# Kernel tuning notes

Hardware: AMD Instinct MI355X
Metric: run time of the kernel (lower is better)

Reference implementation:

```python
import jax, jax.numpy as jnp
import numpy as np

NUM_ITER = 3  # num_itterations

def squash(s):
    # Faithful to the module's (non-standard) squash: out = |s|^2 * s / (1 + |s|^2 * (|s| + 1e-9)).
    # torch sums over dim=-2 of [..., D, 1]; here s is [..., D] so sum over last axis.
    sq = jnp.sum(s * s, axis=-1, keepdims=True)
    norm = jnp.sqrt(sq)
    return sq * s / (1.0 + sq * (norm + 1e-9))

def setup_inputs() -> dict:
    key = jax.random.key(0)
    k1, k2 = jax.random.split(key)
    B, P, N, T, D = 512, 1152, 10, 16, 8
    x = jax.random.normal(k1, (B, P, D), dtype=jnp.float32)          # input capsules
    W = jax.random.normal(k2, (P, N, T, D), dtype=jnp.float32)       # routing transform (torch W with leading 1 dropped)
    return {"x": x, "W": W}

def reference(x, B_unused=None, *, _=None, **__):
    raise RuntimeError('placeholder')

def reference(x, W):
    # prediction u_hat[b,p,n,:] = W[p,n] @ x[b,p]  -> [B, P, N, T]
    pred = jnp.einsum('pntd,bpd->bpnt', W, x)
    B, P, N = pred.shape[0], pred.shape[1], pred.shape[2]
    b_ij = jnp.zeros((B, P, N), dtype=x.dtype)
    v = None
    for i in range(NUM_ITER):
        # torch.tensor(c_ij) detaches the coupling coefficients from the graph
        c = jax.lax.stop_gradient(jax.nn.softmax(b_ij, axis=2))      # softmax over next-caps dim
        s = jnp.einsum('bpn,bpnt->bnt', c, pred)                     # weighted sum over prev caps
        v = squash(s)                                                # [B, N, T]
        if i < NUM_ITER - 1:
            a = jnp.einsum('bpnt,bnt->bpn', pred, v)                 # agreement
            b_ij = b_ij + jnp.mean(a, axis=0, keepdims=True)         # torch mean over batch, keepdim, broadcast-add
    return v[..., None]  # [B, numNextCaps, nextCapsDim, 1] matching torch v_j.squeeze(1)
```

## Files before the change

kernel.cpp:

```cpp
#include <hip/hip_runtime.h>
#include <hip/hip_bf16.h>


typedef __attribute__((ext_vector_type(8))) short bfrag;
typedef __attribute__((ext_vector_type(4))) float f32x4;

constexpr int B_ = 512, P_ = 1152, N_ = 10, NT_ = 160;
constexpr int K1_ = 9216, NKC_ = 288;

__device__ __forceinline__ unsigned short f2bf(float f) {
    unsigned u = __float_as_uint(f);
    return (unsigned short)((u + 0x7fffu + ((u >> 16) & 1u)) >> 16);
}
__device__ __forceinline__ float bf2f(unsigned short s) {
    return __uint_as_float((unsigned)s << 16);
}
__device__ __forceinline__ bfrag mkfrag(f32x4 a, f32x4 b, float c) {
    bfrag f;
    f[0] = (short)f2bf(a.x * c); f[1] = (short)f2bf(a.y * c);
    f[2] = (short)f2bf(a.z * c); f[3] = (short)f2bf(a.w * c);
    f[4] = (short)f2bf(b.x * c); f[5] = (short)f2bf(b.y * c);
    f[6] = (short)f2bf(b.z * c); f[7] = (short)f2bf(b.w * c);
    return f;
}

__global__ __launch_bounds__(256) void k_prep(const float* __restrict__ x,
                                              const float* __restrict__ W,
                                              unsigned short* __restrict__ Xb,
                                              unsigned short* __restrict__ Xga,
                                              unsigned short* __restrict__ Wc,
                                              unsigned short* __restrict__ Wb) {
    const int bid = blockIdx.x, tid = threadIdx.x;
    const int w = tid >> 6, ln = tid & 63, col = ln & 15, q = ln >> 4;
    if (bid < 1152) {
        __shared__ unsigned short tile[64][72];
        const int pd0 = (bid >> 3) * 64, b0 = (bid & 7) * 64;
        const int c0 = tid & 63, r0 = tid >> 6;
#pragma unroll
        for (int i = 0; i < 16; ++i) {
            const int br = i * 4 + r0;
            tile[c0][br] = f2bf(x[(size_t)(b0 + br) * K1_ + pd0 + c0]);
        }
        __syncthreads();
#pragma unroll
        for (int fi = 0; fi < 2; ++fi) {
            const int f = w + fi * 4;
            const int pdblk_l = f & 3, kc_l = f >> 2;
            bfrag fr;
#pragma unroll
            for (int j = 0; j < 8; ++j)
                fr[j] = (short)tile[pdblk_l * 16 + col][kc_l * 32 + q * 8 + j];
            const size_t addr = ((size_t)(((pd0 >> 4) + pdblk_l) * 16 + (b0 >> 5) + kc_l)) * 512 + ln * 8;
            *(bfrag*)(Xga + addr) = fr;
        }
#pragma unroll
        for (int fi = 0; fi < 2; ++fi) {
            const int f = w + fi * 4;
            const int mblk_l = f & 3, kc_l = f >> 2;
            bfrag fr;
#pragma unroll
            for (int j = 0; j < 8; ++j)
                fr[j] = (short)tile[kc_l * 32 + q * 8 + j][mblk_l * 16 + col];
            const size_t addr = ((size_t)(((b0 >> 4) + mblk_l) * NKC_ + (pd0 >> 5) + kc_l)) * 512 + ln * 8;
            *(bfrag*)(Xb + addr) = fr;
        }
    } else if (bid < 1872) {
        const int task = (bid - 1152) * 4 + w;
        const int n = task / NKC_, kc = task % NKC_;
        const int p = kc * 4 + q;
        const float* wr = W + ((size_t)p * NT_ + n * 16 + col) * 8;
        const bfrag f = mkfrag(*(const f32x4*)wr, *(const f32x4*)(wr + 4), 0.1f);
        *(bfrag*)(Wc + ((size_t)(n * NKC_ + kc)) * 512 + ln * 8) = f;
    } else {
        const int idx = (bid - 1872) * 256 + tid;
        const int p = ((idx >> 6) * 16 + (idx & 15)) >> 3, d = idx & 7;
        const int q2 = (idx & 63) >> 4;
        unsigned short* dst = Wb + (size_t)idx * 40;
#pragma unroll
        for (int mt = 0; mt < N_; ++mt)
#pragma unroll
            for (int r = 0; r < 4; ++r)
                dst[mt * 4 + r] = f2bf(W[((size_t)p * NT_ + mt * 16 + q2 * 4 + r) * 8 + d]);
    }
}

__global__ __launch_bounds__(1024) void k_sv(const unsigned short* __restrict__ Xb,
                                             const unsigned short* __restrict__ Wc,
                                             unsigned short* __restrict__ Vt,
                                             float* __restrict__ outp,
                                             int final_it) {
    __shared__ float red[15 * 256];
    const int tid = threadIdx.x;
    const int w = tid >> 6, lane = tid & 63, col = lane & 15, q = lane >> 4;
    const int mblk = blockIdx.x;
    const int n0 = blockIdx.y;

    f32x4 accA = (f32x4){0.f, 0.f, 0.f, 0.f};
    f32x4 accB = (f32x4){0.f, 0.f, 0.f, 0.f};
    const int kc0 = w * 18;
    const unsigned short* Xp = Xb + ((size_t)(mblk * NKC_ + kc0)) * 512 + lane * 8;
    const unsigned short* W0 = Wc + ((size_t)(n0 * NKC_ + kc0)) * 512 + lane * 8;
#pragma unroll 3
    for (int i = 0; i < 9; ++i) {
        const bfrag a0 = *(const bfrag*)Xp;
        const bfrag b0 = *(const bfrag*)W0;
        const bfrag a1 = *(const bfrag*)(Xp + 512);
        const bfrag b1 = *(const bfrag*)(W0 + 512);
        accA = __builtin_amdgcn_mfma_f32_16x16x32_bf16(a0, b0, accA, 0, 0, 0);
        accB = __builtin_amdgcn_mfma_f32_16x16x32_bf16(a1, b1, accB, 0, 0, 0);
        Xp += 1024; W0 += 1024;
    }
    f32x4 acc;
#pragma unroll
    for (int r = 0; r < 4; ++r) acc[r] = accA[r] + accB[r];
    if (w) {
#pragma unroll
        for (int r = 0; r < 4; ++r)
            red[(w - 1) * 256 + r * 64 + q * 16 + col] = acc[r];
    }
    __syncthreads();
    if (w == 0) {
#pragma unroll
        for (int r = 0; r < 4; ++r) {
            const int li = r * 64 + q * 16 + col;
            float s = acc[r];
#pragma unroll
            for (int j = 0; j < 15; ++j) s += red[j * 256 + li];
            float sq = s * s;
            sq += __shfl_xor(sq, 1);
            sq += __shfl_xor(sq, 2);
            sq += __shfl_xor(sq, 4);
            sq += __shfl_xor(sq, 8);
            const float norm = sqrtf(sq);
            const float scale = sq / (1.0f + sq * (norm + 1e-9f));
            const float vv = s * scale;
            const int b = mblk * 16 + q * 4 + r;
            const int nt = n0 * 16 + col;
            if (final_it) outp[(size_t)b * NT_ + nt] = vv;
            else          Vt[(size_t)nt * B_ + b] = f2bf(vv);
        }
    }
}

__global__ __launch_bounds__(256) void k_ga(const unsigned short* __restrict__ Vt,
                                            const unsigned short* __restrict__ Xga,
                                            const unsigned short* __restrict__ Wb,
                                            const float* __restrict__ W,
                                            float* __restrict__ bbar,
                                            unsigned short* __restrict__ Wc,
                                            int accum) {
    __shared__ float bred[3][64][41];
    __shared__ float csm[2][N_];
    const int tid = threadIdx.x;
    const int w = tid >> 6, lane = tid & 63, col = lane & 15, q = lane >> 4;
    const int pdblk = blockIdx.x;
    const int p = (pdblk * 16 + col) >> 3, d = col & 7;

    f32x4 acc[N_];
#pragma unroll
    for (int mt = 0; mt < N_; ++mt) acc[mt] = (f32x4){0.f, 0.f, 0.f, 0.f};

    const int kb0 = w * 4;
#pragma unroll
    for (int kc = kb0; kc < kb0 + 4; ++kc) {
        const bfrag bf = *(const bfrag*)(Xga + ((size_t)(pdblk * 16 + kc)) * 512 + lane * 8);
#pragma unroll
        for (int mt = 0; mt < N_; ++mt) {
            const bfrag af = *(const bfrag*)(Vt + (size_t)(mt * 16 + col) * B_ + kc * 32 + q * 8);
            acc[mt] = __builtin_amdgcn_mfma_f32_16x16x32_bf16(af, bf, acc[mt], 0, 0, 0);
        }
    }
    if (w) {
#pragma unroll
        for (int mt = 0; mt < N_; ++mt)
#pragma unroll
            for (int r = 0; r < 4; ++r)
                bred[w - 1][lane][mt * 4 + r] = acc[mt][r];
    }
    __syncthreads();
    if (w == 0) {
        unsigned short wv[40];
        const unsigned short* ws2 = Wb + ((size_t)(pdblk * 64 + lane)) * 40;
#pragma unroll
        for (int v = 0; v < 40; ++v) wv[v] = ws2[v];
        float part[N_];
#pragma unroll
        for (int mt = 0; mt < N_; ++mt) {
            float s = 0.f;
#pragma unroll
            for (int r = 0; r < 4; ++r) {
                const float h = acc[mt][r] + bred[0][lane][mt * 4 + r]
                              + bred[1][lane][mt * 4 + r] + bred[2][lane][mt * 4 + r];
                s = fmaf(bf2f(wv[mt * 4 + r]), h, s);
            }
            s += __shfl_xor(s, 1);
            s += __shfl_xor(s, 2);
            s += __shfl_xor(s, 4);
            s += __shfl_xor(s, 16);
            s += __shfl_xor(s, 32);
            part[mt] = s;
        }
        if (q == 0 && d == 0) {
            const int pl = col >> 3;
            float bv[N_];
#pragma unroll
            for (int mt = 0; mt < N_; ++mt) {
                bv[mt] = part[mt] * (1.0f / 512.0f);
                if (accum) bv[mt] += bbar[(size_t)p * N_ + mt];
                bbar[(size_t)p * N_ + mt] = bv[mt];
            }
            float m = -1e30f;
#pragma unroll
            for (int mt = 0; mt < N_; ++mt) m = fmaxf(m, bv[mt]);
            float sum = 0.f;
#pragma unroll
            for (int mt = 0; mt < N_; ++mt) { bv[mt] = __expf(bv[mt] - m); sum += bv[mt]; }
            const float inv = 1.f / sum;
#pragma unroll
            for (int mt = 0; mt < N_; ++mt) csm[pl][mt] = bv[mt] * inv;
        }
    }
    __syncthreads();
    const int p0 = pdblk * 2;
#pragma unroll
    for (int task = tid; task < 320; task += 256) {
        const int pl = task / 160, rem = task % 160;
        const int n = rem >> 4, cl = rem & 15;
        const int pp = p0 + pl;
        const float c = csm[pl][n];
        const float* wr = W + ((size_t)pp * NT_ + n * 16 + cl) * 8;
        const size_t addr = ((size_t)(n * NKC_ + (pp >> 2))) * 512 + (pp & 3) * 128 + cl * 8;
        *(bfrag*)(Wc + addr) = mkfrag(*(const f32x4*)wr, *(const f32x4*)(wr + 4), c);
    }
}

extern "C" void kernel_launch(void* const* d_in, const int* in_sizes, int n_in,
                              void* d_out, int out_size, void* d_ws, size_t ws_size,
                              hipStream_t stream) {
    const float* x = (const float*)d_in[0];
    const float* W = (const float*)d_in[1];

    char* wsp = (char*)d_ws;
    float* bbar = (float*)wsp;
    unsigned short* Xb  = (unsigned short*)(wsp + 46080);
    unsigned short* Xga = Xb + (size_t)32 * NKC_ * 512;
    unsigned short* Wc  = Xga + (size_t)576 * 16 * 512;
    unsigned short* Wb  = Wc + (size_t)N_ * NKC_ * 512;
    unsigned short* Vt  = Wb + (size_t)576 * 64 * 40;
    float* outp = (float*)d_out;

    k_prep<<<dim3(2016), dim3(256), 0, stream>>>(x, W, Xb, Xga, Wc, Wb);
    k_sv<<<dim3(32, 10), dim3(1024), 0, stream>>>(Xb, Wc, Vt, outp, 0);
    k_ga<<<dim3(576), dim3(256), 0, stream>>>(Vt, Xga, Wb, W, bbar, Wc, 0);
    k_sv<<<dim3(32, 10), dim3(1024), 0, stream>>>(Xb, Wc, Vt, outp, 0);
    k_ga<<<dim3(576), dim3(256), 0, stream>>>(Vt, Xga, Wb, W, bbar, Wc, 1);
    k_sv<<<dim3(32, 10), dim3(1024), 0, stream>>>(Xb, Wc, Vt, outp, 1);
}
```

Measured before the change: 154.8 us.

## Compute two capsule tiles per k_sv block and pair k_ga blocks with fragment-ordered Vt

k_sv now has each block produce two next-capsule tiles, so one loaded X fragment feeds two MFMAs. This halves the X traffic and the grid size. Vt is written in the MFMA fragment layout, which lets k_ga load A fragments contiguously per lane instead of with strided gathers. k_ga merges two pd-blocks into one 512-thread block, halving the block count. Risks are lower occupancy and parallelism with fewer blocks, plus more shared memory per block.

```diff
diff --git a/kernel.cpp b/kernel.cpp
--- a/kernel.cpp
+++ b/kernel.cpp
@@ -89,43 +89,41 @@
                                              unsigned short* __restrict__ Vt,
                                              float* __restrict__ outp,
                                              int final_it) {
-    __shared__ float red[15 * 256];
+    __shared__ float red[16][2][256];
     const int tid = threadIdx.x;
     const int w = tid >> 6, lane = tid & 63, col = lane & 15, q = lane >> 4;
     const int mblk = blockIdx.x;
-    const int n0 = blockIdx.y;
+    const int n0 = blockIdx.y * 2;
 
     f32x4 accA = (f32x4){0.f, 0.f, 0.f, 0.f};
     f32x4 accB = (f32x4){0.f, 0.f, 0.f, 0.f};
     const int kc0 = w * 18;
     const unsigned short* Xp = Xb + ((size_t)(mblk * NKC_ + kc0)) * 512 + lane * 8;
     const unsigned short* W0 = Wc + ((size_t)(n0 * NKC_ + kc0)) * 512 + lane * 8;
+    const unsigned short* W1 = W0 + (size_t)NKC_ * 512;
 #pragma unroll 3
-    for (int i = 0; i < 9; ++i) {
-        const bfrag a0 = *(const bfrag*)Xp;
+    for (int i = 0; i < 18; ++i) {
+        const bfrag a  = *(const bfrag*)Xp;
         const bfrag b0 = *(const bfrag*)W0;
-        const bfrag a1 = *(const bfrag*)(Xp + 512);
-        const bfrag b1 = *(const bfrag*)(W0 + 512);
-        accA = __builtin_amdgcn_mfma_f32_16x16x32_bf16(a0, b0, accA, 0, 0, 0);
-        accB = __builtin_amdgcn_mfma_f32_16x16x32_bf16(a1, b1, accB, 0, 0, 0);
-        Xp += 1024; W0 += 1024;
-    }
-    f32x4 acc;
-#pragma unroll
-    for (int r = 0; r < 4; ++r) acc[r] = accA[r] + accB[r];
-    if (w) {
-#pragma unroll
-        for (int r = 0; r < 4; ++r)
-            red[(w - 1) * 256 + r * 64 + q * 16 + col] = acc[r];
+        const bfrag b1 = *(const bfrag*)W1;
+        accA = __builtin_amdgcn_mfma_f32_16x16x32_bf16(a, b0, accA, 0, 0, 0);
+        accB = __builtin_amdgcn_mfma_f32_16x16x32_bf16(a, b1, accB, 0, 0, 0);
+        Xp += 512; W0 += 512; W1 += 512;
+    }
+#pragma unroll
+    for (int r = 0; r < 4; ++r) {
+        red[w][0][r * 64 + q * 16 + col] = accA[r];
+        red[w][1][r * 64 + q * 16 + col] = accB[r];
     }
     __syncthreads();
-    if (w == 0) {
+    if (w < 2) {
+        const int mt = n0 + w;
 #pragma unroll
         for (int r = 0; r < 4; ++r) {
             const int li = r * 64 + q * 16 + col;
-            float s = acc[r];
-#pragma unroll
-            for (int j = 0; j < 15; ++j) s += red[j * 256 + li];
+            float s = 0.f;
+#pragma unroll
+            for (int j = 0; j < 16; ++j) s += red[j][w][li];
             float sq = s * s;
             sq += __shfl_xor(sq, 1);
             sq += __shfl_xor(sq, 2);
@@ -135,50 +133,55 @@
             const float scale = sq / (1.0f + sq * (norm + 1e-9f));
             const float vv = s * scale;
             const int b = mblk * 16 + q * 4 + r;
-            const int nt = n0 * 16 + col;
-            if (final_it) outp[(size_t)b * NT_ + nt] = vv;
-            else          Vt[(size_t)nt * B_ + b] = f2bf(vv);
-        }
-    }
-}
-
-__global__ __launch_bounds__(256) void k_ga(const unsigned short* __restrict__ Vt,
+            if (final_it) {
+                outp[(size_t)b * NT_ + mt * 16 + col] = vv;
+            } else {
+                const int b5 = b & 31;
+                Vt[((size_t)((mblk >> 1) * N_ + mt)) * 512
+                   + ((b5 >> 3) * 16 + col) * 8 + (b5 & 7)] = f2bf(vv);
+            }
+        }
+    }
+}
+
+__global__ __launch_bounds__(512) void k_ga(const unsigned short* __restrict__ Vt,
                                             const unsigned short* __restrict__ Xga,
                                             const unsigned short* __restrict__ Wb,
                                             const float* __restrict__ W,
                                             float* __restrict__ bbar,
                                             unsigned short* __restrict__ Wc,
                                             int accum) {
-    __shared__ float bred[3][64][41];
-    __shared__ float csm[2][N_];
+    __shared__ float bred[2][3][64][41];
+    __shared__ float csm[4][N_];
     const int tid = threadIdx.x;
     const int w = tid >> 6, lane = tid & 63, col = lane & 15, q = lane >> 4;
-    const int pdblk = blockIdx.x;
+    const int half = w >> 2, wl = w & 3;
+    const int pdblk = blockIdx.x * 2 + half;
     const int p = (pdblk * 16 + col) >> 3, d = col & 7;
 
     f32x4 acc[N_];
 #pragma unroll
     for (int mt = 0; mt < N_; ++mt) acc[mt] = (f32x4){0.f, 0.f, 0.f, 0.f};
 
-    const int kb0 = w * 4;
+    const int kb0 = wl * 4;
 #pragma unroll
     for (int kc = kb0; kc < kb0 + 4; ++kc) {
         const bfrag bf = *(const bfrag*)(Xga + ((size_t)(pdblk * 16 + kc)) * 512 + lane * 8);
 #pragma unroll
         for (int mt = 0; mt < N_; ++mt) {
-            const bfrag af = *(const bfrag*)(Vt + (size_t)(mt * 16 + col) * B_ + kc * 32 + q * 8);
+            const bfrag af = *(const bfrag*)(Vt + ((size_t)(kc * N_ + mt)) * 512 + lane * 8);
             acc[mt] = __builtin_amdgcn_mfma_f32_16x16x32_bf16(af, bf, acc[mt], 0, 0, 0);
         }
     }
-    if (w) {
+    if (wl) {
 #pragma unroll
         for (int mt = 0; mt < N_; ++mt)
 #pragma unroll
             for (int r = 0; r < 4; ++r)
-                bred[w - 1][lane][mt * 4 + r] = acc[mt][r];
+                bred[half][wl - 1][lane][mt * 4 + r] = acc[mt][r];
     }
     __syncthreads();
-    if (w == 0) {
+    if (wl == 0) {
         unsigned short wv[40];
         const unsigned short* ws2 = Wb + ((size_t)(pdblk * 64 + lane)) * 40;
 #pragma unroll
@@ -189,8 +192,9 @@
             float s = 0.f;
 #pragma unroll
             for (int r = 0; r < 4; ++r) {
-                const float h = acc[mt][r] + bred[0][lane][mt * 4 + r]
-                              + bred[1][lane][mt * 4 + r] + bred[2][lane][mt * 4 + r];
+                const float h = acc[mt][r] + bred[half][0][lane][mt * 4 + r]
+                              + bred[half][1][lane][mt * 4 + r]
+                              + bred[half][2][lane][mt * 4 + r];
                 s = fmaf(bf2f(wv[mt * 4 + r]), h, s);
             }
             s += __shfl_xor(s, 1);
@@ -217,13 +221,13 @@
             for (int mt = 0; mt < N_; ++mt) { bv[mt] = __expf(bv[mt] - m); sum += bv[mt]; }
             const float inv = 1.f / sum;
 #pragma unroll
-            for (int mt = 0; mt < N_; ++mt) csm[pl][mt] = bv[mt] * inv;
+            for (int mt = 0; mt < N_; ++mt) csm[half * 2 + pl][mt] = bv[mt] * inv;
         }
     }
     __syncthreads();
-    const int p0 = pdblk * 2;
-#pragma unroll
-    for (int task = tid; task < 320; task += 256) {
+    const int p0 = blockIdx.x * 4;
+#pragma unroll
+    for (int task = tid; task < 640; task += 512) {
         const int pl = task / 160, rem = task % 160;
         const int n = rem >> 4, cl = rem & 15;
         const int pp = p0 + pl;
@@ -250,9 +254,9 @@
     float* outp = (float*)d_out;
 
     k_prep<<<dim3(2016), dim3(256), 0, stream>>>(x, W, Xb, Xga, Wc, Wb);
-    k_sv<<<dim3(32, 10), dim3(1024), 0, stream>>>(Xb, Wc, Vt, outp, 0);
-    k_ga<<<dim3(576), dim3(256), 0, stream>>>(Vt, Xga, Wb, W, bbar, Wc, 0);
-    k_sv<<<dim3(32, 10), dim3(1024), 0, stream>>>(Xb, Wc, Vt, outp, 0);
-    k_ga<<<dim3(576), dim3(256), 0, stream>>>(Vt, Xga, Wb, W, bbar, Wc, 1);
-    k_sv<<<dim3(32, 10), dim3(1024), 0, stream>>>(Xb, Wc, Vt, outp, 1);
-}
+    k_sv<<<dim3(32, 5), dim3(1024), 0, stream>>>(Xb, Wc, Vt, outp, 0);
+    k_ga<<<dim3(288), dim3(512), 0, stream>>>(Vt, Xga, Wb, W, bbar, Wc, 0);
+    k_sv<<<dim3(32, 5), dim3(1024), 0, stream>>>(Xb, Wc, Vt, outp, 0);
+    k_ga<<<dim3(288), dim3(512), 0, stream>>>(Vt, Xga, Wb, W, bbar, Wc, 1);
+    k_sv<<<dim3(32, 5), dim3(1024), 0, stream>>>(Xb, Wc, Vt, outp, 1);
+}
```

Result: faster. 136.1 us (-12.0%).
